# Kernel optimization log

Measured on AMD Instinct MI355X. Metric: run time of the kernel, lower is better.

## Reference

```python
import jax, jax.numpy as jnp
import numpy as np

RADIUS = 0.4
NSAMPLE = 32
EPS = 1e-5  # BatchNorm2d default eps


def setup_inputs() -> dict:
    key = jax.random.key(0)
    ks = jax.random.split(key, 16)
    B, N, C, P = 16, 4096, 128, 1024
    inp = {
        "xyz": jax.random.uniform(ks[0], (B, N, 3), dtype=jnp.float32),
        "features": jax.random.normal(ks[1], (B, C, N), dtype=jnp.float32),
        "num_points": P,
    }
    dims = [C + 3, 128, 128, 256]  # in_channel = mlps[0] + 3, then mlps[1:]
    for i in range(3):
        cin, cout = dims[i], dims[i + 1]
        inp[f"w{i}"] = jax.random.normal(ks[2 + 4 * i], (cout, cin), jnp.float32) * (1.0 / np.sqrt(cin))
        inp[f"b{i}"] = jnp.zeros((cout,), jnp.float32)
        inp[f"g{i}"] = jnp.ones((cout,), jnp.float32)
        inp[f"beta{i}"] = jnp.zeros((cout,), jnp.float32)
    return inp


def _ball_query_group(xyz, new_xyz, features):
    """QueryAndGroup: ball query (first NSAMPLE in-radius indices, padded with
    the first hit), gather, subtract center, concat [rel_xyz; feats]."""
    N = xyz.shape[1]
    # squared distances [B, P, N]
    d2 = jnp.sum((new_xyz[:, :, None, :] - xyz[:, None, :, :]) ** 2, axis=-1)
    cand = jnp.where(d2 < RADIUS * RADIUS,
                     jnp.arange(N, dtype=jnp.int32)[None, None, :], N)
    idx = jnp.sort(cand, axis=-1)[:, :, :NSAMPLE]          # first hits, in order
    idx = jnp.where(idx == N, idx[:, :, :1], idx)           # pad with first hit
    # gather per batch: xyz [N,3] indexed by idx [P,S] -> [P,S,3]
    grouped_xyz = jax.vmap(lambda p, i: p[i])(xyz, idx) - new_xyz[:, :, None, :]
    # features [C,N] indexed along N -> [C,P,S]
    grouped_feat = jax.vmap(lambda f, i: f[:, i])(features, idx)
    # [B, 3+C, P, S]
    return jnp.concatenate([grouped_xyz.transpose(0, 3, 1, 2), grouped_feat], axis=1), idx


def _conv_bn_relu(x, w, b, g, beta):
    # 1x1 Conv2d: pointwise channel mix over [B, Cin, P, S]
    x = jnp.einsum('oi,bips->bops', w, x) + b[None, :, None, None]
    # BatchNorm2d, training mode (batch statistics over B,P,S per channel)
    m = jnp.mean(x, axis=(0, 2, 3), keepdims=True)
    v = jnp.mean((x - m) ** 2, axis=(0, 2, 3), keepdims=True)
    x = g[None, :, None, None] * (x - m) * jax.lax.rsqrt(v + EPS) + beta[None, :, None, None]
    return jax.nn.relu(x)


def reference(xyz, features, num_points,
              w0, b0, g0, beta0, w1, b1, g1, beta1, w2, b2, g2, beta2):
    B = xyz.shape[0]
    # use_fps=False: sample_idxs = arange(num_points) per batch
    sample_idxs = jnp.tile(jnp.arange(num_points, dtype=jnp.int32)[None], (B, 1))
    new_xyz = xyz[:, :num_points]                    # gather_operation with arange
    x, _ = _ball_query_group(xyz, new_xyz, features)  # [B, 131, P, S]
    for w, b, g, bt in ((w0, b0, g0, beta0), (w1, b1, g1, beta1), (w2, b2, g2, beta2)):
        x = _conv_bn_relu(x, w, b, g, bt)
    new_features = jnp.max(x, axis=-1)               # max-pool over nsample
    return new_xyz, new_features, sample_idxs
```

## Files before the change

kernel.cpp:

```cpp
#include <hip/hip_runtime.h>

#define BB 16
#define NN 4096
#define CC 128
#define PP 1024
#define SS 32
#define MM (BB*PP*SS)
#define NBLK 8192
#define OFF_NF 49152
#define OFF_SI 4243456

typedef unsigned short u16;
typedef unsigned int u32;
typedef __attribute__((ext_vector_type(8))) short short8v;
typedef __attribute__((ext_vector_type(4))) float f32x4;

__device__ __forceinline__ float b2f(u16 u) {
    union { float f; unsigned i; } x; x.i = ((unsigned)u) << 16; return x.f;
}
__device__ __forceinline__ u16 f2b(float f) {
    union { float f; unsigned i; } x; x.f = f;
    unsigned r = x.i + 0x7fffu + ((x.i >> 16) & 1u);
    return (u16)(r >> 16);
}
__device__ __forceinline__ float2 act2(u32 u, float2 s0, float2 s1) {
    union { float f; unsigned i; } a, b;
    a.i = u << 16; b.i = u & 0xffff0000u;
    return make_float2(fmaxf(fmaf(s0.x, a.f, s0.y), 0.f),
                       fmaxf(fmaf(s1.x, b.f, s1.y), 0.f));
}
__device__ __forceinline__ u32 packbf(float flo, float fhi) {
    union { float f; unsigned i; } x0, x1; x0.f = flo; x1.f = fhi;
    return __builtin_amdgcn_perm(x1.i, x0.i, 0x07060302u);
}
__device__ __forceinline__ u32 packbf_rtne(float flo, float fhi) {
    union { float f; unsigned i; } x0, x1; x0.f = flo; x1.f = fhi;
    u32 r0 = x0.i + 0x7fffu + ((x0.i >> 16) & 1u);
    u32 r1 = x1.i + 0x7fffu + ((x1.i >> 16) & 1u);
    return __builtin_amdgcn_perm(r1, r0, 0x07060302u);
}
__device__ __forceinline__ u32 act_pack(u32 u, float2 s0, float2 s1) {
    float2 f = act2(u, s0, s1);
    return packbf(f.x, f.y);
}
__device__ __forceinline__ short8v as_s8(uint4 v) {
    union { uint4 u; short8v s; } x; x.u = v; return x.s;
}

#define MFMA16(a,b,c) __builtin_amdgcn_mfma_f32_16x16x32_bf16(a,b,c,0,0,0)

__global__ void k_init(const float* __restrict__ xyz, const float* __restrict__ w0,
                       const float* __restrict__ w1, const float* __restrict__ w2,
                       float* __restrict__ out, float* __restrict__ w0t,
                       u16* __restrict__ w0b, u16* __restrict__ w1b,
                       u16* __restrict__ w2b) {
    int i = blockIdx.x * 256 + threadIdx.x;
    if (i < 49152) {
        int b = i / 3072, r = i % 3072;
        out[i] = xyz[b * 12288 + r];
        return;
    }
    int j = i - 49152;
    if (j < 16384) { out[OFF_SI + j] = (float)(j & 1023); return; }
    int e = j - 16384;
    if (e < 384) { w0t[e] = w0[(e & 127) * 131 + (e >> 7)]; return; }
    int f = e - 384;
    if (f < 16384) { w0b[f] = f2b(w0[(f >> 7) * 131 + 3 + (f & 127)]); return; }
    int h = f - 16384;
    if (h < 16384) { w1b[h] = f2b(w1[h]); return; }
    int k2 = h - 16384;
    if (k2 < 32768) { w2b[k2] = f2b(w2[k2]); }
}

__global__ __launch_bounds__(256) void k_ballquery(const float* __restrict__ xyz,
                                                   int* __restrict__ oidx,
                                                   float* __restrict__ relx,
                                                   float* __restrict__ rely,
                                                   float* __restrict__ relz) {
    __shared__ float sx[NN], sy[NN], sz[NN];
    int t = threadIdx.x, w = t >> 6, lane = t & 63;
    int b = blockIdx.x >> 8;
    int p = (blockIdx.x & 255) * 4 + w;
    const float* xb = xyz + (long)b * NN * 3;
    for (int i = t; i < NN; i += 256) {
        sx[i] = xb[3 * i]; sy[i] = xb[3 * i + 1]; sz[i] = xb[3 * i + 2];
    }
    __syncthreads();
    const float R2 = (float)(0.4 * 0.4);
    float cx = sx[p], cy = sy[p], cz = sz[p];
    int o = (b * PP + p) * SS;
    int cnt = 0, firstn = 0;
    float fdx = 0.f, fdy = 0.f, fdz = 0.f;
    for (int c = 0; c < 64 && cnt < 32; ++c) {
        int n = c * 64 + lane;
        float dx = __fsub_rn(sx[n], cx);
        float dy = __fsub_rn(sy[n], cy);
        float dz = __fsub_rn(sz[n], cz);
        float d2 = __fadd_rn(__fadd_rn(__fmul_rn(dx, dx), __fmul_rn(dy, dy)),
                             __fmul_rn(dz, dz));
        bool hit = d2 < R2;
        unsigned long long mask = __ballot(hit);
        if (mask) {
            if (cnt == 0) {
                int fl = __ffsll(mask) - 1;
                firstn = c * 64 + fl;
                fdx = __shfl(dx, fl); fdy = __shfl(dy, fl); fdz = __shfl(dz, fl);
            }
            int pos = cnt + __popcll(mask & ((1ull << lane) - 1ull));
            if (hit && pos < 32) {
                oidx[o + pos] = n;
                relx[o + pos] = dx; rely[o + pos] = dy; relz[o + pos] = dz;
            }
            cnt += __popcll(mask);
        }
    }
    if (lane < 32 && lane >= cnt) {
        oidx[o + lane] = firstn;
        relx[o + lane] = fdx; rely[o + lane] = fdy; relz[o + lane] = fdz;
    }
}

__global__ __launch_bounds__(256) void k_f1(const float* __restrict__ feat,
                                            const u16* __restrict__ w0b,
                                            float* __restrict__ F1) {
    __shared__ uint4 abuf[64 * 17];
    int t = threadIdx.x;
    int w = t >> 6, lane = t & 63, q = lane >> 4, l16 = lane & 15;
    int cb = (w & 1) * 64, wm0 = (w >> 1) * 32;
    short8v bf[4][4];
#pragma unroll
    for (int ct = 0; ct < 4; ++ct)
#pragma unroll
        for (int k0 = 0; k0 < 4; ++k0)
            bf[ct][k0] = *(const short8v*)(w0b + (cb + ct * 16 + l16) * 128 + k0 * 32 + q * 8);
    int nl = t & 63, cg = t >> 6;
    const float* fcol = feat + (long)(blockIdx.x >> 6) * (128 * 4096)
                             + (long)(blockIdx.x & 63) * 64 + nl;
#pragma unroll
    for (int pp = 0; pp < 4; ++pp) {
        int oct = cg + 4 * pp;
        float v[8];
#pragma unroll
        for (int r = 0; r < 8; ++r) v[r] = fcol[(long)(oct * 8 + r) * 4096];
        uint4 ov;
        ov.x = packbf_rtne(v[0], v[1]); ov.y = packbf_rtne(v[2], v[3]);
        ov.z = packbf_rtne(v[4], v[5]); ov.w = packbf_rtne(v[6], v[7]);
        abuf[nl * 17 + ((oct + nl) & 15)] = ov;
    }
    __syncthreads();
    f32x4 acc[2][4];
#pragma unroll
    for (int mt = 0; mt < 2; ++mt)
#pragma unroll
        for (int ct = 0; ct < 4; ++ct) acc[mt][ct] = (f32x4){0.f, 0.f, 0.f, 0.f};
#pragma unroll
    for (int mt = 0; mt < 2; ++mt) {
        int row = wm0 + mt * 16 + l16;
#pragma unroll
        for (int k0 = 0; k0 < 4; ++k0) {
            uint4 vv = abuf[row * 17 + ((k0 * 4 + q + row) & 15)];
            short8v af = as_s8(vv);
#pragma unroll
            for (int ct = 0; ct < 4; ++ct)
                acc[mt][ct] = MFMA16(af, bf[ct][k0], acc[mt][ct]);
        }
    }
    long nbase = (long)blockIdx.x * 64;
#pragma unroll
    for (int mt = 0; mt < 2; ++mt)
#pragma unroll
        for (int ct = 0; ct < 4; ++ct)
#pragma unroll
            for (int r = 0; r < 4; ++r)
                F1[(nbase + wm0 + mt * 16 + q * 4 + r) * 128 + cb + ct * 16 + l16]
                    = acc[mt][ct][r];
}

__global__ __launch_bounds__(256) void k_y0(const float* __restrict__ relx,
                                            const float* __restrict__ rely,
                                            const float* __restrict__ relz,
                                            const float* __restrict__ w0t,
                                            const float* __restrict__ F1,
                                            const int* __restrict__ idx,
                                            u16* __restrict__ y0,
                                            float* __restrict__ part,
                                            float* __restrict__ partq) {
    int t = threadIdx.x, w = t >> 6, lane = t & 63;
    long m0 = (long)blockIdx.x * 64;
    int c0 = 2 * lane;
    float wx0 = w0t[c0],       wx1 = w0t[c0 + 1];
    float wy0 = w0t[128 + c0], wy1 = w0t[128 + c0 + 1];
    float wz0 = w0t[256 + c0], wz1 = w0t[256 + c0 + 1];
    float s1a = 0.f, s1b = 0.f, s2a = 0.f, s2b = 0.f;
    u32* yo = (u32*)y0;
#pragma unroll 4
    for (int i = 0; i < 16; ++i) {
        long m = m0 + w + 4 * i;
        int b = (int)(m >> 15);
        int id = idx[m];
        float rx = relx[m], ry = rely[m], rz = relz[m];
        float2 f = *(const float2*)(F1 + ((long)(b * NN + id)) * 128 + c0);
        float v0 = fmaf(wx0, rx, fmaf(wy0, ry, fmaf(wz0, rz, f.x)));
        float v1 = fmaf(wx1, rx, fmaf(wy1, ry, fmaf(wz1, rz, f.y)));
        yo[m * 64 + lane] = packbf_rtne(v0, v1);
        s1a += v0; s2a = fmaf(v0, v0, s2a);
        s1b += v1; s2b = fmaf(v1, v1, s2b);
    }
    __shared__ float r1[128][4], r2[128][4];
    r1[c0][w] = s1a; r1[c0 + 1][w] = s1b;
    r2[c0][w] = s2a; r2[c0 + 1][w] = s2b;
    __syncthreads();
    if (t < 128) {
        float a1 = r1[t][0] + r1[t][1] + r1[t][2] + r1[t][3];
        float a2 = r2[t][0] + r2[t][1] + r2[t][2] + r2[t][3];
        part [(long)t * NBLK + blockIdx.x] = a1;
        partq[(long)t * NBLK + blockIdx.x] = a2;
    }
}

__global__ void k_bnfin(const float* __restrict__ part, const float* __restrict__ partq,
                        const float* __restrict__ g, const float* __restrict__ beta,
                        float* __restrict__ st, int nblk) {
    int co = blockIdx.x, t = threadIdx.x;
    const float* p1 = part + (long)co * NBLK;
    const float* p2 = partq + (long)co * NBLK;
    float s1 = 0.f, s2 = 0.f;
    for (int j = t; j < nblk; j += 256) { s1 += p1[j]; s2 += p2[j]; }
    __shared__ float r1[256], r2[256];
    r1[t] = s1; r2[t] = s2; __syncthreads();
    for (int off = 128; off > 0; off >>= 1) {
        if (t < off) { r1[t] += r1[t + off]; r2[t] += r2[t + off]; }
        __syncthreads();
    }
    if (t == 0) {
        const float inv = 1.f / (float)MM;
        float mean = r1[0] * inv;
        float var = r2[0] * inv - mean * mean;
        float sc = g[co] * rsqrtf(var + 1e-5f);
        st[2 * co] = sc;
        st[2 * co + 1] = fmaf(-mean, sc, beta[co]);
    }
}

__global__ __launch_bounds__(256, 3) void k_conv1(u16* __restrict__ y,
                                                  const u16* __restrict__ w1b,
                                                  const float* __restrict__ st0,
                                                  float* __restrict__ part,
                                                  float* __restrict__ partq) {
    __shared__ uint4 abuf[2][64 * 17];
    __shared__ float2 sst[128];
    __shared__ float sredA[4][64], sredB[4][64];
    int t = threadIdx.x;
    if (t < 128) sst[t] = ((const float2*)st0)[t];
    int w = t >> 6, lane = t & 63, q = lane >> 4, l16 = lane & 15;
    int wm0 = (w >> 1) * 32, cb = (w & 1) * 64;
    short8v bf[4][4];
#pragma unroll
    for (int ct = 0; ct < 4; ++ct)
#pragma unroll
        for (int k0 = 0; k0 < 4; ++k0)
            bf[ct][k0] = *(const short8v*)(w1b + (cb + ct * 16 + l16) * 128 + k0 * 32 + q * 8);
    __syncthreads();
    long m0b = (long)blockIdx.x * 512;
    float s1[4] = {0.f, 0.f, 0.f, 0.f}, s2[4] = {0.f, 0.f, 0.f, 0.f};
    int sr = t >> 4, sc16 = t & 15;
    for (int c = 0; c < 8; ++c) {
        long m0 = m0b + c * 64;
        uint4* ab = abuf[c & 1];
        const uint4* gsrc = (const uint4*)y;
#pragma unroll
        for (int p = 0; p < 4; ++p) {
            int r = p * 16 + sr;
            uint4 d = gsrc[(m0 + r) * 16 + sc16];
            uint4 o;
            o.x = act_pack(d.x, sst[sc16 * 8 + 0], sst[sc16 * 8 + 1]);
            o.y = act_pack(d.y, sst[sc16 * 8 + 2], sst[sc16 * 8 + 3]);
            o.z = act_pack(d.z, sst[sc16 * 8 + 4], sst[sc16 * 8 + 5]);
            o.w = act_pack(d.w, sst[sc16 * 8 + 6], sst[sc16 * 8 + 7]);
            ab[r * 17 + ((sc16 + r) & 15)] = o;
        }
        __syncthreads();
        f32x4 acc[2][4];
#pragma unroll
        for (int mt = 0; mt < 2; ++mt)
#pragma unroll
            for (int ct = 0; ct < 4; ++ct) acc[mt][ct] = (f32x4){0.f, 0.f, 0.f, 0.f};
#pragma unroll
        for (int mt = 0; mt < 2; ++mt) {
            int row = wm0 + mt * 16 + l16;
#pragma unroll
            for (int k0 = 0; k0 < 4; ++k0) {
                uint4 v = ab[row * 17 + ((k0 * 4 + q + row) & 15)];
                short8v af = as_s8(v);
#pragma unroll
                for (int ct = 0; ct < 4; ++ct)
                    acc[mt][ct] = MFMA16(af, bf[ct][k0], acc[mt][ct]);
            }
        }
#pragma unroll
        for (int mt = 0; mt < 2; ++mt)
#pragma unroll
            for (int ct = 0; ct < 4; ++ct)
#pragma unroll
                for (int r = 0; r < 4; ++r) {
                    float v = acc[mt][ct][r];
                    y[(m0 + wm0 + mt * 16 + q * 4 + r) * 128 + cb + ct * 16 + l16] = f2b(v);
                    s1[ct] += v; s2[ct] = fmaf(v, v, s2[ct]);
                }
    }
#pragma unroll
    for (int ct = 0; ct < 4; ++ct) {
        float a = s1[ct], b = s2[ct];
        a += __shfl_xor(a, 16); a += __shfl_xor(a, 32);
        b += __shfl_xor(b, 16); b += __shfl_xor(b, 32);
        if (lane < 16) { sredA[w][ct * 16 + l16] = a; sredB[w][ct * 16 + l16] = b; }
    }
    __syncthreads();
    if (t < 128) {
        int h = t >> 6, cl = t & 63;
        part [(long)t * NBLK + blockIdx.x] = sredA[h][cl] + sredA[h + 2][cl];
        partq[(long)t * NBLK + blockIdx.x] = sredB[h][cl] + sredB[h + 2][cl];
    }
}

__global__ __launch_bounds__(256) void k_conv2pool(const u16* __restrict__ y1,
                                                   const u16* __restrict__ w2b,
                                                   const float* __restrict__ st1,
                                                   float* __restrict__ rawmax,
                                                   float* __restrict__ rawmin,
                                                   float* __restrict__ part,
                                                   float* __restrict__ partq) {
    __shared__ uint4 abuf[2][64 * 17];
    __shared__ float2 sst[128];
    __shared__ float sredA[4][64], sredB[4][64];
    int t = threadIdx.x;
    if (t < 128) sst[t] = ((const float2*)st1)[t];
    int w = t >> 6, lane = t & 63, q = lane >> 4, l16 = lane & 15;
    int cb = w * 64;
    short8v bf[4][4];
#pragma unroll
    for (int ct = 0; ct < 4; ++ct)
#pragma unroll
        for (int k0 = 0; k0 < 4; ++k0)
            bf[ct][k0] = *(const short8v*)(w2b + (cb + ct * 16 + l16) * 128 + k0 * 32 + q * 8);
    __syncthreads();
    long m0b = (long)blockIdx.x * 512;
    int sr = t >> 4, sc16 = t & 15;
    float s1[4] = {0.f, 0.f, 0.f, 0.f}, s2[4] = {0.f, 0.f, 0.f, 0.f};
    for (int c = 0; c < 8; ++c) {
        long m0 = m0b + c * 64;
        uint4* ab = abuf[c & 1];
        const uint4* gsrc = (const uint4*)y1;
#pragma unroll
        for (int p = 0; p < 4; ++p) {
            int r = p * 16 + sr;
            uint4 d = gsrc[(m0 + r) * 16 + sc16];
            uint4 o;
            o.x = act_pack(d.x, sst[sc16 * 8 + 0], sst[sc16 * 8 + 1]);
            o.y = act_pack(d.y, sst[sc16 * 8 + 2], sst[sc16 * 8 + 3]);
            o.z = act_pack(d.z, sst[sc16 * 8 + 4], sst[sc16 * 8 + 5]);
            o.w = act_pack(d.w, sst[sc16 * 8 + 6], sst[sc16 * 8 + 7]);
            ab[r * 17 + ((sc16 + r) & 15)] = o;
        }
        __syncthreads();
        f32x4 acc[4][4];
#pragma unroll
        for (int mt = 0; mt < 4; ++mt)
#pragma unroll
            for (int ct = 0; ct < 4; ++ct) acc[mt][ct] = (f32x4){0.f, 0.f, 0.f, 0.f};
#pragma unroll
        for (int mt = 0; mt < 4; ++mt) {
            int row = mt * 16 + l16;
#pragma unroll
            for (int k0 = 0; k0 < 4; ++k0) {
                uint4 v = ab[row * 17 + ((k0 * 4 + q + row) & 15)];
                short8v af = as_s8(v);
#pragma unroll
                for (int ct = 0; ct < 4; ++ct)
                    acc[mt][ct] = MFMA16(af, bf[ct][k0], acc[mt][ct]);
            }
        }
#pragma unroll
        for (int ct = 0; ct < 4; ++ct) {
#pragma unroll
            for (int g = 0; g < 2; ++g) {
                f32x4 a0 = acc[2 * g][ct], a1 = acc[2 * g + 1][ct];
                s1[ct] += a0[0] + a0[1] + a0[2] + a0[3] + a1[0] + a1[1] + a1[2] + a1[3];
                s2[ct] = fmaf(a0[0], a0[0], s2[ct]); s2[ct] = fmaf(a0[1], a0[1], s2[ct]);
                s2[ct] = fmaf(a0[2], a0[2], s2[ct]); s2[ct] = fmaf(a0[3], a0[3], s2[ct]);
                s2[ct] = fmaf(a1[0], a1[0], s2[ct]); s2[ct] = fmaf(a1[1], a1[1], s2[ct]);
                s2[ct] = fmaf(a1[2], a1[2], s2[ct]); s2[ct] = fmaf(a1[3], a1[3], s2[ct]);
                float mx = fmaxf(fmaxf(fmaxf(a0[0], a0[1]), fmaxf(a0[2], a0[3])),
                                 fmaxf(fmaxf(a1[0], a1[1]), fmaxf(a1[2], a1[3])));
                float mn = fminf(fminf(fminf(a0[0], a0[1]), fminf(a0[2], a0[3])),
                                 fminf(fminf(a1[0], a1[1]), fminf(a1[2], a1[3])));
                mx = fmaxf(mx, __shfl_xor(mx, 16)); mx = fmaxf(mx, __shfl_xor(mx, 32));
                mn = fminf(mn, __shfl_xor(mn, 16)); mn = fminf(mn, __shfl_xor(mn, 32));
                if (lane < 16) {
                    long bp = (long)blockIdx.x * 16 + c * 2 + g;
                    rawmax[bp * 256 + cb + ct * 16 + l16] = mx;
                    rawmin[bp * 256 + cb + ct * 16 + l16] = mn;
                }
            }
        }
    }
#pragma unroll
    for (int ct = 0; ct < 4; ++ct) {
        float a = s1[ct], b = s2[ct];
        a += __shfl_xor(a, 16); a += __shfl_xor(a, 32);
        b += __shfl_xor(b, 16); b += __shfl_xor(b, 32);
        if (lane < 16) { sredA[w][ct * 16 + l16] = a; sredB[w][ct * 16 + l16] = b; }
    }
    __syncthreads();
    {
        part [(long)t * NBLK + blockIdx.x] = sredA[t >> 6][t & 63];
        partq[(long)t * NBLK + blockIdx.x] = sredB[t >> 6][t & 63];
    }
}

__global__ void k_final(const float* __restrict__ rawmax, const float* __restrict__ rawmin,
                        const float* __restrict__ st2, float* __restrict__ out) {
    __shared__ float tile[32][33];
    int b = blockIdx.x >> 8;
    int p0 = ((blockIdx.x >> 3) & 31) * 32;
    int c0 = (blockIdx.x & 7) * 32;
    int j = threadIdx.x & 31, i0 = threadIdx.x >> 5;
    float sc = st2[2 * (c0 + j)], sh = st2[2 * (c0 + j) + 1];
#pragma unroll
    for (int rr = 0; rr < 4; ++rr) {
        int i = i0 + rr * 8;
        long idx = ((long)(b * 1024 + p0 + i)) * 256 + c0 + j;
        float v = sc > 0.f ? fmaf(sc, rawmax[idx], sh) : fmaf(sc, rawmin[idx], sh);
        tile[i][j] = fmaxf(v, 0.f);
    }
    __syncthreads();
#pragma unroll
    for (int rr = 0; rr < 4; ++rr) {
        int i = i0 + rr * 8;
        out[OFF_NF + (long)b * 262144 + (c0 + i) * 1024 + p0 + j] = tile[j][i];
    }
}

extern "C" void kernel_launch(void* const* d_in, const int* in_sizes, int n_in,
                              void* d_out, int out_size, void* d_ws, size_t ws_size,
                              hipStream_t stream) {
    (void)in_sizes; (void)n_in; (void)out_size; (void)ws_size;
    const float* xyz  = (const float*)d_in[0];
    const float* feat = (const float*)d_in[1];
    const float* w0   = (const float*)d_in[3];
    const float* g0   = (const float*)d_in[5];
    const float* be0  = (const float*)d_in[6];
    const float* w1   = (const float*)d_in[7];
    const float* g1   = (const float*)d_in[9];
    const float* be1  = (const float*)d_in[10];
    const float* w2   = (const float*)d_in[11];
    const float* g2   = (const float*)d_in[13];
    const float* be2  = (const float*)d_in[14];
    float* out = (float*)d_out;

    char* ws = (char*)d_ws;
    size_t off = 0;
    auto alloc = [&](size_t bytes) -> void* {
        void* p = ws + off;
        off = (off + bytes + 4095) & ~(size_t)4095;
        return p;
    };
    int*   idx    = (int*)  alloc((size_t)MM * 4);
    float* relx   = (float*)alloc((size_t)MM * 4);
    float* rely   = (float*)alloc((size_t)MM * 4);
    float* relz   = (float*)alloc((size_t)MM * 4);
    float* w0t    = (float*)alloc(3 * 128 * 4);
    u16*   w0b    = (u16*)  alloc(128 * 128 * 2);
    u16*   w1b    = (u16*)  alloc(128 * 128 * 2);
    u16*   w2b    = (u16*)  alloc(256 * 128 * 2);
    float* st0    = (float*)alloc(128 * 2 * 4);
    float* st1    = (float*)alloc(128 * 2 * 4);
    float* st2    = (float*)alloc(256 * 2 * 4);
    float* part   = (float*)alloc((size_t)256 * NBLK * 4);
    float* partq  = (float*)alloc((size_t)256 * NBLK * 4);
    float* F1     = (float*)alloc((size_t)BB * NN * 128 * 4);
    float* rawmax = (float*)alloc((size_t)BB * PP * 256 * 4);
    float* rawmin = (float*)alloc((size_t)BB * PP * 256 * 4);
    u16*   bufA   = (u16*)  alloc((size_t)MM * 128 * 2);

    k_init<<<514, 256, 0, stream>>>(xyz, w0, w1, w2, out, w0t, w0b, w1b, w2b);
    k_ballquery<<<4096, 256, 0, stream>>>(xyz, idx, relx, rely, relz);
    k_f1<<<1024, 256, 0, stream>>>(feat, w0b, F1);
    k_y0<<<NBLK, 256, 0, stream>>>(relx, rely, relz, w0t, F1, idx, bufA, part, partq);
    k_bnfin<<<128, 256, 0, stream>>>(part, partq, g0, be0, st0, NBLK);
    k_conv1<<<1024, 256, 0, stream>>>(bufA, w1b, st0, part, partq);
    k_bnfin<<<128, 256, 0, stream>>>(part, partq, g1, be1, st1, 1024);
    k_conv2pool<<<1024, 256, 0, stream>>>(bufA, w2b, st1, rawmax, rawmin, part, partq);
    k_bnfin<<<256, 256, 0, stream>>>(part, partq, g2, be2, st2, 1024);
    k_final<<<4096, 256, 0, stream>>>(rawmax, rawmin, st2, out);
}
```

Measured before the change: 329.9 us.

## Compute BN0 stats algebraically from per-point hit counts; fuse y0 gather into conv1

Removes the materialized y0 buffer. The first BatchNorm statistics are now obtained algebraically: ball query accumulates per-source-point hit counts and weighted relative-xyz sums via atomics plus per-wave rel-xyz moments, and a small reduction over F1 combines them into the mean and variance. The conv1 kernel then recomputes y0 on the fly from F1, idx and rel-xyz, applies BN+ReLU and runs the MFMA GEMM. This cuts a large bf16 write/read pass at the cost of global atomics in ball query and reassociated variance arithmetic (E[x^2]-m^2 in fp32).

After: 521.3 us. 1.58x slower.

```diff
diff --git a/kernel.cpp b/kernel.cpp
--- a/kernel.cpp
+++ b/kernel.cpp
@@ -53,7 +53,7 @@
                        const float* __restrict__ w1, const float* __restrict__ w2,
                        float* __restrict__ out, float* __restrict__ w0t,
                        u16* __restrict__ w0b, u16* __restrict__ w1b,
-                       u16* __restrict__ w2b) {
+                       u16* __restrict__ w2b, float* __restrict__ cntw) {
     int i = blockIdx.x * 256 + threadIdx.x;
     if (i < 49152) {
         int b = i / 3072, r = i % 3072;
@@ -69,14 +69,18 @@
     int h = f - 16384;
     if (h < 16384) { w1b[h] = f2b(w1[h]); return; }
     int k2 = h - 16384;
-    if (k2 < 32768) { w2b[k2] = f2b(w2[k2]); }
+    if (k2 < 32768) { w2b[k2] = f2b(w2[k2]); return; }
+    int z = k2 - 32768;
+    if (z < 262144) { cntw[z] = 0.f; }
 }
 
 __global__ __launch_bounds__(256) void k_ballquery(const float* __restrict__ xyz,
                                                    int* __restrict__ oidx,
                                                    float* __restrict__ relx,
                                                    float* __restrict__ rely,
-                                                   float* __restrict__ relz) {
+                                                   float* __restrict__ relz,
+                                                   float* __restrict__ cntw,
+                                                   float* __restrict__ rpart) {
     __shared__ float sx[NN], sy[NN], sz[NN];
     int t = threadIdx.x, w = t >> 6, lane = t & 63;
     int b = blockIdx.x >> 8;
@@ -86,11 +90,17 @@
         sx[i] = xb[3 * i]; sy[i] = xb[3 * i + 1]; sz[i] = xb[3 * i + 2];
     }
     __syncthreads();
+    float* cntp = cntw;
+    float* wxp = cntw + 65536;
+    float* wyp = cntw + 2 * 65536;
+    float* wzp = cntw + 3 * 65536;
     const float R2 = (float)(0.4 * 0.4);
     float cx = sx[p], cy = sy[p], cz = sz[p];
     int o = (b * PP + p) * SS;
     int cnt = 0, firstn = 0;
     float fdx = 0.f, fdy = 0.f, fdz = 0.f;
+    float srx = 0.f, sry = 0.f, srz = 0.f;
+    float sxx = 0.f, syy = 0.f, szz = 0.f, sxy = 0.f, sxz = 0.f, syz = 0.f;
     for (int c = 0; c < 64 && cnt < 32; ++c) {
         int n = c * 64 + lane;
         float dx = __fsub_rn(sx[n], cx);
@@ -110,13 +120,44 @@
             if (hit && pos < 32) {
                 oidx[o + pos] = n;
                 relx[o + pos] = dx; rely[o + pos] = dy; relz[o + pos] = dz;
+                int gn = b * NN + n;
+                atomicAdd(&cntp[gn], 1.f);
+                atomicAdd(&wxp[gn], dx); atomicAdd(&wyp[gn], dy); atomicAdd(&wzp[gn], dz);
+                srx += dx; sry += dy; srz += dz;
+                sxx = fmaf(dx, dx, sxx); syy = fmaf(dy, dy, syy); szz = fmaf(dz, dz, szz);
+                sxy = fmaf(dx, dy, sxy); sxz = fmaf(dx, dz, sxz); syz = fmaf(dy, dz, syz);
             }
             cnt += __popcll(mask);
         }
     }
-    if (lane < 32 && lane >= cnt) {
+    int stored = cnt < 32 ? cnt : 32;
+    if (lane < 32 && lane >= stored) {
         oidx[o + lane] = firstn;
         relx[o + lane] = fdx; rely[o + lane] = fdy; relz[o + lane] = fdz;
+    }
+    if (lane == 0 && stored < 32) {
+        float pad = (float)(32 - stored);
+        int gn = b * NN + firstn;
+        atomicAdd(&cntp[gn], pad);
+        atomicAdd(&wxp[gn], pad * fdx); atomicAdd(&wyp[gn], pad * fdy);
+        atomicAdd(&wzp[gn], pad * fdz);
+        srx += pad * fdx; sry += pad * fdy; srz += pad * fdz;
+        sxx += pad * fdx * fdx; syy += pad * fdy * fdy; szz += pad * fdz * fdz;
+        sxy += pad * fdx * fdy; sxz += pad * fdx * fdz; syz += pad * fdy * fdz;
+    }
+#pragma unroll
+    for (int d = 1; d < 64; d <<= 1) {
+        srx += __shfl_xor(srx, d); sry += __shfl_xor(sry, d); srz += __shfl_xor(srz, d);
+        sxx += __shfl_xor(sxx, d); syy += __shfl_xor(syy, d); szz += __shfl_xor(szz, d);
+        sxy += __shfl_xor(sxy, d); sxz += __shfl_xor(sxz, d); syz += __shfl_xor(syz, d);
+    }
+    if (lane == 0) {
+        int wid = blockIdx.x * 4 + w;
+        rpart[0 * 16384 + wid] = srx; rpart[1 * 16384 + wid] = sry;
+        rpart[2 * 16384 + wid] = srz; rpart[3 * 16384 + wid] = sxx;
+        rpart[4 * 16384 + wid] = syy; rpart[5 * 16384 + wid] = szz;
+        rpart[6 * 16384 + wid] = sxy; rpart[7 * 16384 + wid] = sxz;
+        rpart[8 * 16384 + wid] = syz;
     }
 }
 
@@ -176,45 +217,191 @@
                     = acc[mt][ct][r];
 }
 
-__global__ __launch_bounds__(256) void k_y0(const float* __restrict__ relx,
-                                            const float* __restrict__ rely,
-                                            const float* __restrict__ relz,
-                                            const float* __restrict__ w0t,
-                                            const float* __restrict__ F1,
-                                            const int* __restrict__ idx,
-                                            u16* __restrict__ y0,
-                                            float* __restrict__ part,
-                                            float* __restrict__ partq) {
+__global__ __launch_bounds__(256) void k_st0part(const float* __restrict__ F1,
+                                                 const float* __restrict__ cntw,
+                                                 float* __restrict__ p5) {
     int t = threadIdx.x, w = t >> 6, lane = t & 63;
-    long m0 = (long)blockIdx.x * 64;
     int c0 = 2 * lane;
-    float wx0 = w0t[c0],       wx1 = w0t[c0 + 1];
-    float wy0 = w0t[128 + c0], wy1 = w0t[128 + c0 + 1];
-    float wz0 = w0t[256 + c0], wz1 = w0t[256 + c0 + 1];
-    float s1a = 0.f, s1b = 0.f, s2a = 0.f, s2b = 0.f;
-    u32* yo = (u32*)y0;
-#pragma unroll 4
-    for (int i = 0; i < 16; ++i) {
-        long m = m0 + w + 4 * i;
-        int b = (int)(m >> 15);
-        int id = idx[m];
-        float rx = relx[m], ry = rely[m], rz = relz[m];
-        float2 f = *(const float2*)(F1 + ((long)(b * NN + id)) * 128 + c0);
-        float v0 = fmaf(wx0, rx, fmaf(wy0, ry, fmaf(wz0, rz, f.x)));
-        float v1 = fmaf(wx1, rx, fmaf(wy1, ry, fmaf(wz1, rz, f.y)));
-        yo[m * 64 + lane] = packbf_rtne(v0, v1);
-        s1a += v0; s2a = fmaf(v0, v0, s2a);
-        s1b += v1; s2b = fmaf(v1, v1, s2b);
-    }
-    __shared__ float r1[128][4], r2[128][4];
-    r1[c0][w] = s1a; r1[c0 + 1][w] = s1b;
-    r2[c0][w] = s2a; r2[c0 + 1][w] = s2b;
+    const float* cntp = cntw;
+    const float* wxp = cntw + 65536;
+    const float* wyp = cntw + 2 * 65536;
+    const float* wzp = cntw + 3 * 65536;
+    float p1a = 0.f, p1b = 0.f, p2a = 0.f, p2b = 0.f;
+    float pxa = 0.f, pxb = 0.f, pya = 0.f, pyb = 0.f, pza = 0.f, pzb = 0.f;
+    int base = blockIdx.x * 256 + w;
+    for (int i = 0; i < 64; ++i) {
+        int n = base + 4 * i;
+        float cn = cntp[n], wxn = wxp[n], wyn = wyp[n], wzn = wzp[n];
+        float2 f = *(const float2*)(F1 + (long)n * 128 + c0);
+        p1a = fmaf(cn, f.x, p1a);        p1b = fmaf(cn, f.y, p1b);
+        p2a = fmaf(cn * f.x, f.x, p2a);  p2b = fmaf(cn * f.y, f.y, p2b);
+        pxa = fmaf(wxn, f.x, pxa);       pxb = fmaf(wxn, f.y, pxb);
+        pya = fmaf(wyn, f.x, pya);       pyb = fmaf(wyn, f.y, pyb);
+        pza = fmaf(wzn, f.x, pza);       pzb = fmaf(wzn, f.y, pzb);
+    }
+    __shared__ float red[5][128][4];
+    red[0][c0][w] = p1a; red[0][c0 + 1][w] = p1b;
+    red[1][c0][w] = p2a; red[1][c0 + 1][w] = p2b;
+    red[2][c0][w] = pxa; red[2][c0 + 1][w] = pxb;
+    red[3][c0][w] = pya; red[3][c0 + 1][w] = pyb;
+    red[4][c0][w] = pza; red[4][c0 + 1][w] = pzb;
     __syncthreads();
     if (t < 128) {
-        float a1 = r1[t][0] + r1[t][1] + r1[t][2] + r1[t][3];
-        float a2 = r2[t][0] + r2[t][1] + r2[t][2] + r2[t][3];
-        part [(long)t * NBLK + blockIdx.x] = a1;
-        partq[(long)t * NBLK + blockIdx.x] = a2;
+#pragma unroll
+        for (int k = 0; k < 5; ++k)
+            p5[k * 32768 + t * 256 + blockIdx.x]
+                = red[k][t][0] + red[k][t][1] + red[k][t][2] + red[k][t][3];
+    }
+}
+
+__global__ void k_st0fin(const float* __restrict__ p5, const float* __restrict__ rpart,
+                         const float* __restrict__ w0t, const float* __restrict__ g0,
+                         const float* __restrict__ be0, float* __restrict__ st0) {
+    __shared__ float sred[9][16];
+    __shared__ float scal[9];
+    int t = threadIdx.x;
+    if (t < 144) {
+        int k = t >> 4, s = t & 15;
+        const float* rp = rpart + k * 16384 + s * 1024;
+        float a = 0.f;
+        for (int j = 0; j < 1024; ++j) a += rp[j];
+        sred[k][s] = a;
+    }
+    __syncthreads();
+    if (t < 9) {
+        float a = 0.f;
+        for (int s = 0; s < 16; ++s) a += sred[t][s];
+        scal[t] = a;
+    }
+    __syncthreads();
+    if (t < 128) {
+        float P1 = 0.f, P2 = 0.f, PX = 0.f, PY = 0.f, PZ = 0.f;
+        const float* b0 = p5 + t * 256;
+        for (int j = 0; j < 256; ++j) {
+            P1 += b0[j];
+            P2 += b0[32768 + j];
+            PX += b0[2 * 32768 + j];
+            PY += b0[3 * 32768 + j];
+            PZ += b0[4 * 32768 + j];
+        }
+        float wx = w0t[t], wy = w0t[128 + t], wz = w0t[256 + t];
+        float S1 = P1 + wx * scal[0] + wy * scal[1] + wz * scal[2];
+        float S2 = P2 + 2.f * (wx * PX + wy * PY + wz * PZ)
+                 + wx * wx * scal[3] + wy * wy * scal[4] + wz * wz * scal[5]
+                 + 2.f * (wx * wy * scal[6] + wx * wz * scal[7] + wy * wz * scal[8]);
+        const float inv = 1.f / (float)MM;
+        float mean = S1 * inv;
+        float var = S2 * inv - mean * mean;
+        float sc = g0[t] * rsqrtf(var + 1e-5f);
+        st0[2 * t] = sc;
+        st0[2 * t + 1] = fmaf(-mean, sc, be0[t]);
+    }
+}
+
+__global__ __launch_bounds__(256, 2) void k_conv1f(const float* __restrict__ F1,
+                                                   const int* __restrict__ idx,
+                                                   const float* __restrict__ relx,
+                                                   const float* __restrict__ rely,
+                                                   const float* __restrict__ relz,
+                                                   const float* __restrict__ w0t,
+                                                   const u16* __restrict__ w1b,
+                                                   const float* __restrict__ st0,
+                                                   u16* __restrict__ y1,
+                                                   float* __restrict__ part,
+                                                   float* __restrict__ partq) {
+    __shared__ uint4 abuf[2][64 * 17];
+    __shared__ float2 sst[128];
+    __shared__ float sredA[4][64], sredB[4][64];
+    int t = threadIdx.x;
+    if (t < 128) sst[t] = ((const float2*)st0)[t];
+    int w = t >> 6, lane = t & 63, q = lane >> 4, l16 = lane & 15;
+    int wm0 = (w >> 1) * 32, cb = (w & 1) * 64;
+    short8v bf[4][4];
+#pragma unroll
+    for (int ct = 0; ct < 4; ++ct)
+#pragma unroll
+        for (int k0 = 0; k0 < 4; ++k0)
+            bf[ct][k0] = *(const short8v*)(w1b + (cb + ct * 16 + l16) * 128 + k0 * 32 + q * 8);
+    int sr = t >> 4, sc16 = t & 15;
+    float wxr[8], wyr[8], wzr[8];
+#pragma unroll
+    for (int j = 0; j < 8; ++j) {
+        wxr[j] = w0t[sc16 * 8 + j];
+        wyr[j] = w0t[128 + sc16 * 8 + j];
+        wzr[j] = w0t[256 + sc16 * 8 + j];
+    }
+    __syncthreads();
+    long m0b = (long)blockIdx.x * 512;
+    float s1[4] = {0.f, 0.f, 0.f, 0.f}, s2[4] = {0.f, 0.f, 0.f, 0.f};
+    for (int c = 0; c < 8; ++c) {
+        long m0 = m0b + c * 64;
+        uint4* ab = abuf[c & 1];
+#pragma unroll
+        for (int p = 0; p < 4; ++p) {
+            int r = p * 16 + sr;
+            long m = m0 + r;
+            int id = idx[m];
+            int b = (int)(m >> 15);
+            float rx = relx[m], ry = rely[m], rz = relz[m];
+            const float* fr = F1 + ((long)(b * NN + id)) * 128 + sc16 * 8;
+            float4 fa = *(const float4*)fr;
+            float4 fb = *(const float4*)(fr + 4);
+            float v[8] = {fa.x, fa.y, fa.z, fa.w, fb.x, fb.y, fb.z, fb.w};
+            u32 od[4];
+#pragma unroll
+            for (int j = 0; j < 4; ++j) {
+                float y0a = fmaf(wxr[2 * j], rx, fmaf(wyr[2 * j], ry,
+                             fmaf(wzr[2 * j], rz, v[2 * j])));
+                float y0b = fmaf(wxr[2 * j + 1], rx, fmaf(wyr[2 * j + 1], ry,
+                             fmaf(wzr[2 * j + 1], rz, v[2 * j + 1])));
+                float2 ss0 = sst[sc16 * 8 + 2 * j], ss1 = sst[sc16 * 8 + 2 * j + 1];
+                float a0 = fmaxf(fmaf(ss0.x, y0a, ss0.y), 0.f);
+                float a1 = fmaxf(fmaf(ss1.x, y0b, ss1.y), 0.f);
+                od[j] = packbf(a0, a1);
+            }
+            ab[r * 17 + ((sc16 + r) & 15)] = make_uint4(od[0], od[1], od[2], od[3]);
+        }
+        __syncthreads();
+        f32x4 acc[2][4];
+#pragma unroll
+        for (int mt = 0; mt < 2; ++mt)
+#pragma unroll
+            for (int ct = 0; ct < 4; ++ct) acc[mt][ct] = (f32x4){0.f, 0.f, 0.f, 0.f};
+#pragma unroll
+        for (int mt = 0; mt < 2; ++mt) {
+            int row = wm0 + mt * 16 + l16;
+#pragma unroll
+            for (int k0 = 0; k0 < 4; ++k0) {
+                uint4 v = ab[row * 17 + ((k0 * 4 + q + row) & 15)];
+                short8v af = as_s8(v);
+#pragma unroll
+                for (int ct = 0; ct < 4; ++ct)
+                    acc[mt][ct] = MFMA16(af, bf[ct][k0], acc[mt][ct]);
+            }
+        }
+#pragma unroll
+        for (int mt = 0; mt < 2; ++mt)
+#pragma unroll
+            for (int ct = 0; ct < 4; ++ct)
+#pragma unroll
+                for (int r = 0; r < 4; ++r) {
+                    float v = acc[mt][ct][r];
+                    y1[(m0 + wm0 + mt * 16 + q * 4 + r) * 128 + cb + ct * 16 + l16] = f2b(v);
+                    s1[ct] += v; s2[ct] = fmaf(v, v, s2[ct]);
+                }
+    }
+#pragma unroll
+    for (int ct = 0; ct < 4; ++ct) {
+        float a = s1[ct], b = s2[ct];
+        a += __shfl_xor(a, 16); a += __shfl_xor(a, 32);
+        b += __shfl_xor(b, 16); b += __shfl_xor(b, 32);
+        if (lane < 16) { sredA[w][ct * 16 + l16] = a; sredB[w][ct * 16 + l16] = b; }
+    }
+    __syncthreads();
+    if (t < 128) {
+        int h = t >> 6, cl = t & 63;
+        part [(long)t * NBLK + blockIdx.x] = sredA[h][cl] + sredA[h + 2][cl];
+        partq[(long)t * NBLK + blockIdx.x] = sredB[h][cl] + sredB[h + 2][cl];
     }
 }
 
@@ -239,87 +426,6 @@
         float sc = g[co] * rsqrtf(var + 1e-5f);
         st[2 * co] = sc;
         st[2 * co + 1] = fmaf(-mean, sc, beta[co]);
-    }
-}
-
-__global__ __launch_bounds__(256, 3) void k_conv1(u16* __restrict__ y,
-                                                  const u16* __restrict__ w1b,
-                                                  const float* __restrict__ st0,
-                                                  float* __restrict__ part,
-                                                  float* __restrict__ partq) {
-    __shared__ uint4 abuf[2][64 * 17];
-    __shared__ float2 sst[128];
-    __shared__ float sredA[4][64], sredB[4][64];
-    int t = threadIdx.x;
-    if (t < 128) sst[t] = ((const float2*)st0)[t];
-    int w = t >> 6, lane = t & 63, q = lane >> 4, l16 = lane & 15;
-    int wm0 = (w >> 1) * 32, cb = (w & 1) * 64;
-    short8v bf[4][4];
-#pragma unroll
-    for (int ct = 0; ct < 4; ++ct)
-#pragma unroll
-        for (int k0 = 0; k0 < 4; ++k0)
-            bf[ct][k0] = *(const short8v*)(w1b + (cb + ct * 16 + l16) * 128 + k0 * 32 + q * 8);
-    __syncthreads();
-    long m0b = (long)blockIdx.x * 512;
-    float s1[4] = {0.f, 0.f, 0.f, 0.f}, s2[4] = {0.f, 0.f, 0.f, 0.f};
-    int sr = t >> 4, sc16 = t & 15;
-    for (int c = 0; c < 8; ++c) {
-        long m0 = m0b + c * 64;
-        uint4* ab = abuf[c & 1];
-        const uint4* gsrc = (const uint4*)y;
-#pragma unroll
-        for (int p = 0; p < 4; ++p) {
-            int r = p * 16 + sr;
-            uint4 d = gsrc[(m0 + r) * 16 + sc16];
-            uint4 o;
-            o.x = act_pack(d.x, sst[sc16 * 8 + 0], sst[sc16 * 8 + 1]);
-            o.y = act_pack(d.y, sst[sc16 * 8 + 2], sst[sc16 * 8 + 3]);
-            o.z = act_pack(d.z, sst[sc16 * 8 + 4], sst[sc16 * 8 + 5]);
-            o.w = act_pack(d.w, sst[sc16 * 8 + 6], sst[sc16 * 8 + 7]);
-            ab[r * 17 + ((sc16 + r) & 15)] = o;
-        }
-        __syncthreads();
-        f32x4 acc[2][4];
-#pragma unroll
-        for (int mt = 0; mt < 2; ++mt)
-#pragma unroll
-            for (int ct = 0; ct < 4; ++ct) acc[mt][ct] = (f32x4){0.f, 0.f, 0.f, 0.f};
-#pragma unroll
-        for (int mt = 0; mt < 2; ++mt) {
-            int row = wm0 + mt * 16 + l16;
-#pragma unroll
-            for (int k0 = 0; k0 < 4; ++k0) {
-                uint4 v = ab[row * 17 + ((k0 * 4 + q + row) & 15)];
-                short8v af = as_s8(v);
-#pragma unroll
-                for (int ct = 0; ct < 4; ++ct)
-                    acc[mt][ct] = MFMA16(af, bf[ct][k0], acc[mt][ct]);
-            }
-        }
-#pragma unroll
-        for (int mt = 0; mt < 2; ++mt)
-#pragma unroll
-            for (int ct = 0; ct < 4; ++ct)
-#pragma unroll
-                for (int r = 0; r < 4; ++r) {
-                    float v = acc[mt][ct][r];
-                    y[(m0 + wm0 + mt * 16 + q * 4 + r) * 128 + cb + ct * 16 + l16] = f2b(v);
-                    s1[ct] += v; s2[ct] = fmaf(v, v, s2[ct]);
-                }
-    }
-#pragma unroll
-    for (int ct = 0; ct < 4; ++ct) {
-        float a = s1[ct], b = s2[ct];
-        a += __shfl_xor(a, 16); a += __shfl_xor(a, 32);
-        b += __shfl_xor(b, 16); b += __shfl_xor(b, 32);
-        if (lane < 16) { sredA[w][ct * 16 + l16] = a; sredB[w][ct * 16 + l16] = b; }
-    }
-    __syncthreads();
-    if (t < 128) {
-        int h = t >> 6, cl = t & 63;
-        part [(long)t * NBLK + blockIdx.x] = sredA[h][cl] + sredA[h + 2][cl];
-        partq[(long)t * NBLK + blockIdx.x] = sredB[h][cl] + sredB[h + 2][cl];
     }
 }
 
@@ -476,6 +582,9 @@
     float* st0    = (float*)alloc(128 * 2 * 4);
     float* st1    = (float*)alloc(128 * 2 * 4);
     float* st2    = (float*)alloc(256 * 2 * 4);
+    float* cntw   = (float*)alloc((size_t)4 * 65536 * 4);
+    float* rpart  = (float*)alloc((size_t)9 * 16384 * 4);
+    float* p5     = (float*)alloc((size_t)5 * 128 * 256 * 4);
     float* part   = (float*)alloc((size_t)256 * NBLK * 4);
     float* partq  = (float*)alloc((size_t)256 * NBLK * 4);
     float* F1     = (float*)alloc((size_t)BB * NN * 128 * 4);
@@ -483,12 +592,13 @@
     float* rawmin = (float*)alloc((size_t)BB * PP * 256 * 4);
     u16*   bufA   = (u16*)  alloc((size_t)MM * 128 * 2);
 
-    k_init<<<514, 256, 0, stream>>>(xyz, w0, w1, w2, out, w0t, w0b, w1b, w2b);
-    k_ballquery<<<4096, 256, 0, stream>>>(xyz, idx, relx, rely, relz);
+    k_init<<<1538, 256, 0, stream>>>(xyz, w0, w1, w2, out, w0t, w0b, w1b, w2b, cntw);
+    k_ballquery<<<4096, 256, 0, stream>>>(xyz, idx, relx, rely, relz, cntw, rpart);
     k_f1<<<1024, 256, 0, stream>>>(feat, w0b, F1);
-    k_y0<<<NBLK, 256, 0, stream>>>(relx, rely, relz, w0t, F1, idx, bufA, part, partq);
-    k_bnfin<<<128, 256, 0, stream>>>(part, partq, g0, be0, st0, NBLK);
-    k_conv1<<<1024, 256, 0, stream>>>(bufA, w1b, st0, part, partq);
+    k_st0part<<<256, 256, 0, stream>>>(F1, cntw, p5);
+    k_st0fin<<<1, 256, 0, stream>>>(p5, rpart, w0t, g0, be0, st0);
+    k_conv1f<<<1024, 256, 0, stream>>>(F1, idx, relx, rely, relz, w0t, w1b, st0,
+                                       bufA, part, partq);
     k_bnfin<<<128, 256, 0, stream>>>(part, partq, g1, be1, st1, 1024);
     k_conv2pool<<<1024, 256, 0, stream>>>(bufA, w2b, st1, rawmax, rawmin, part, partq);
     k_bnfin<<<256, 256, 0, stream>>>(part, partq, g2, be2, st2, 1024);
```
